# Performance work log

Measured on AMD Instinct MI355X. Metric: run time of the kernel, lower is better.

Reference implementation:

```python
import jax, jax.numpy as jnp
import numpy as np

DIM = 96
EPS = 1e-5

def setup_inputs() -> dict:
    key = jax.random.key(0)
    k1, k2, k3, k4 = jax.random.split(key, 4)
    x = jax.random.normal(k1, (2, DIM, 32, 64, 64), dtype=jnp.float32)
    # LayerNorm(8*dim) params and Linear(8*dim -> 2*dim, bias=False) weight
    gamma = jnp.ones((8 * DIM,), dtype=jnp.float32)
    beta = jnp.zeros((8 * DIM,), dtype=jnp.float32)
    w_red = jax.random.normal(k2, (8 * DIM, 2 * DIM), dtype=jnp.float32) * (1.0 / np.sqrt(8 * DIM))
    return {"x": x, "gamma": gamma, "beta": beta, "w_red": w_red}


def _patch_merge(x, gamma, beta, w_red):
    B, C, D, H, W = x.shape
    # pad trailing spatial dims to even (static shapes -> python ifs are fine)
    if (D % 2) or (H % 2) or (W % 2):
        x = jnp.pad(x, ((0, 0), (0, 0), (0, D % 2), (0, H % 2), (0, W % 2)))
    x = jnp.transpose(x, (0, 2, 3, 4, 1))  # B, D, H, W, C
    # gather the 8 octant sub-lattices and concat on channel
    parts = [x[:, d::2, h::2, w::2, :]
             for d in (0, 1) for h in (0, 1) for w in (0, 1)]
    # torch order: x0..x7 indexed by (d,h,w) bits with d slowest -> matches loop order
    y = jnp.concatenate(parts, axis=-1)  # B, D/2, H/2, W/2, 8C
    # LayerNorm over last dim
    mu = jnp.mean(y, axis=-1, keepdims=True)
    var = jnp.mean(jnp.square(y - mu), axis=-1, keepdims=True)
    y = (y - mu) * jax.lax.rsqrt(var + EPS) * gamma + beta
    # Linear 8C -> 2C, no bias
    y = jnp.einsum('bdhwc,co->bdhwo', y, w_red)
    return jnp.transpose(y, (0, 4, 1, 2, 3))  # B, 2C, D/2, H/2, W/2


def reference(x, gamma, beta, w_red):
    return _patch_merge(x, gamma, beta, w_red)
```

## Files before the change

kernel.cpp:

```cpp
#include <hip/hip_runtime.h>

typedef __attribute__((ext_vector_type(8))) short short8;
typedef __attribute__((ext_vector_type(4))) float float4v;

__device__ __forceinline__ unsigned short f2bf(float f) {
  unsigned int u = __float_as_uint(f);
  u += 0x7fffu + ((u >> 16) & 1u);
  return (unsigned short)(u >> 16);
}
__device__ __forceinline__ float bf2f(unsigned short h) {
  return __uint_as_float(((unsigned int)h) << 16);
}

__global__ __launch_bounds__(256)
void prep_kernel(const float* __restrict__ w_red, const float* __restrict__ gamma,
                 const float* __restrict__ beta, unsigned short* __restrict__ w_bf,
                 float* __restrict__ colsum, float* __restrict__ bias) {
  const int n = blockIdx.x;
  const int t = threadIdx.x;
  float cs = 0.f, bs = 0.f;
#pragma unroll
  for (int j = 0; j < 3; ++j) {
    int kp = j * 256 + t;
    int ko = (kp & 7) * 96 + (kp >> 3);
    float w = w_red[(size_t)ko * 192 + n];
    unsigned short v = f2bf(gamma[ko] * w);
    w_bf[(size_t)n * 768 + kp] = v;
    cs += bf2f(v);
    bs += beta[ko] * w;
  }
#pragma unroll
  for (int off = 1; off < 64; off <<= 1) {
    cs += __shfl_xor(cs, off, 64);
    bs += __shfl_xor(bs, off, 64);
  }
  __shared__ float red[2][4];
  const int wave = t >> 6;
  if ((t & 63) == 0) { red[0][wave] = cs; red[1][wave] = bs; }
  __syncthreads();
  if (t == 0) {
    colsum[n] = red[0][0] + red[0][1] + red[0][2] + red[0][3];
    bias[n]   = red[1][0] + red[1][1] + red[1][2] + red[1][3];
  }
}

__global__ __launch_bounds__(256, 6)
void pm_kernel(const float* __restrict__ x, const unsigned short* __restrict__ w_bf,
               const float* __restrict__ colsum, const float* __restrict__ bias,
               float* __restrict__ out) {
  __shared__ __align__(16) unsigned short Y[16][776];
  __shared__ float4 part4[4][8];
  __shared__ float smu[16], srs[16];

  const int tid = threadIdx.x;
  const int bid = blockIdx.x;
  const int b  = bid >> 10;
  const int dz = (bid >> 6) & 15;
  const int hy = (bid >> 1) & 31;
  const int wh = bid & 1;

  const float* xb = x + (size_t)b * 12582912u + (size_t)dz * 8192u
                      + (size_t)hy * 128u + wh * 32;

  const int r0 = tid >> 3;
  const int c0 = r0 >> 2;
  const int di = (r0 >> 1) & 1;
  const int hi = r0 & 1;
  const int w0 = (tid & 7) << 2;
  const float* xp = xb + (size_t)c0 * 131072u + di * 4096 + hi * 64 + w0;

  float4 v[12];
#pragma unroll
  for (int it = 0; it < 12; ++it)
    v[it] = *(const float4*)(xp + (size_t)it * 1048576u);

  const int lane = tid & 63;
  const int wave = tid >> 6;
  const int lrow = lane & 15;
  const int lq   = lane >> 4;

  const int wx0 = (tid & 7) << 1;
  const int k00 = c0 * 8 + di * 4 + hi * 2;
  float sum0 = 0.f, sq0 = 0.f, sum1 = 0.f, sq1 = 0.f;
#pragma unroll
  for (int it = 0; it < 12; ++it) {
    float4 vv = v[it];
    unsigned int p01 = (unsigned int)f2bf(vv.x) | ((unsigned int)f2bf(vv.y) << 16);
    unsigned int p23 = (unsigned int)f2bf(vv.z) | ((unsigned int)f2bf(vv.w) << 16);
    int k0 = it * 64 + k00;
    *(unsigned int*)&Y[wx0][k0]     = p01;
    *(unsigned int*)&Y[wx0 + 1][k0] = p23;
    sum0 += vv.x + vv.y;  sq0 += vv.x * vv.x + vv.y * vv.y;
    sum1 += vv.z + vv.w;  sq1 += vv.z * vv.z + vv.w * vv.w;
  }
#pragma unroll
  for (int off = 8; off < 64; off <<= 1) {
    sum0 += __shfl_xor(sum0, off, 64);  sq0 += __shfl_xor(sq0, off, 64);
    sum1 += __shfl_xor(sum1, off, 64);  sq1 += __shfl_xor(sq1, off, 64);
  }
  if (lane < 8) part4[wave][lane] = make_float4(sum0, sq0, sum1, sq1);

  const unsigned short* wrow[3];
#pragma unroll
  for (int t3 = 0; t3 < 3; ++t3)
    wrow[t3] = w_bf + (size_t)((wave * 3 + t3) * 16 + lrow) * 768 + lq * 8;
  short8 b0[3], b1[3];
#pragma unroll
  for (int t3 = 0; t3 < 3; ++t3) b0[t3] = *(const short8*)(wrow[t3]);
#pragma unroll
  for (int t3 = 0; t3 < 3; ++t3) b1[t3] = *(const short8*)(wrow[t3] + 32);

  __syncthreads();

  if (tid < 16) {
    int l = tid >> 1, odd = tid & 1;
    float s = 0.f, q = 0.f;
#pragma unroll
    for (int w = 0; w < 4; ++w) {
      float4 p = part4[w][l];
      s += odd ? p.z : p.x;
      q += odd ? p.w : p.y;
    }
    float mu  = s * (1.f / 768.f);
    float var = q * (1.f / 768.f) - mu * mu;
    smu[tid] = mu;
    srs[tid] = rsqrtf(var + 1e-5f);
  }

  float cs_n[3], bi_n[3];
#pragma unroll
  for (int t3 = 0; t3 < 3; ++t3) {
    int ng = (wave * 3 + t3) * 16 + lrow;
    cs_n[t3] = colsum[ng];
    bi_n[t3] = bias[ng];
  }

  __syncthreads();

  float4v acc[3];
#pragma unroll
  for (int j2 = 0; j2 < 3; ++j2)
#pragma unroll
    for (int r = 0; r < 4; ++r) acc[j2][r] = 0.f;

  for (int kc = 0; kc < 24; ++kc) {
    int kn = (kc + 2 <= 23) ? kc + 2 : 23;
    short8 b2[3];
#pragma unroll
    for (int t3 = 0; t3 < 3; ++t3) b2[t3] = *(const short8*)(wrow[t3] + kn * 32);
    short8 a0 = *(const short8*)&Y[lrow][kc * 32 + lq * 8];
#pragma unroll
    for (int t3 = 0; t3 < 3; ++t3)
      acc[t3] = __builtin_amdgcn_mfma_f32_16x16x32_bf16(a0, b0[t3], acc[t3], 0, 0, 0);
#pragma unroll
    for (int t3 = 0; t3 < 3; ++t3) { b0[t3] = b1[t3]; b1[t3] = b2[t3]; }
  }

  float4 mu4 = *(const float4*)&smu[lq * 4];
  float4 rs4 = *(const float4*)&srs[lq * 4];
  float* ob = out + (size_t)b * 3145728u + (size_t)dz * 1024u
                  + (size_t)hy * 32u + wh * 16 + lq * 4;
#pragma unroll
  for (int t3 = 0; t3 < 3; ++t3) {
    int ng = (wave * 3 + t3) * 16 + lrow;
    float4 vv;
    vv.x = rs4.x * (acc[t3][0] - mu4.x * cs_n[t3]) + bi_n[t3];
    vv.y = rs4.y * (acc[t3][1] - mu4.y * cs_n[t3]) + bi_n[t3];
    vv.z = rs4.z * (acc[t3][2] - mu4.z * cs_n[t3]) + bi_n[t3];
    vv.w = rs4.w * (acc[t3][3] - mu4.w * cs_n[t3]) + bi_n[t3];
    *(float4*)(ob + (size_t)ng * 16384u) = vv;
  }
}

extern "C" void kernel_launch(void* const* d_in, const int* in_sizes, int n_in,
                              void* d_out, int out_size, void* d_ws, size_t ws_size,
                              hipStream_t stream) {
  const float* x     = (const float*)d_in[0];
  const float* gamma = (const float*)d_in[1];
  const float* beta  = (const float*)d_in[2];
  const float* w_red = (const float*)d_in[3];
  float* out = (float*)d_out;

  unsigned short* w_bf = (unsigned short*)d_ws;
  float* colsum = (float*)((char*)d_ws + 294912);
  float* bias   = colsum + 192;

  prep_kernel<<<dim3(192), dim3(256), 0, stream>>>(w_red, gamma, beta, w_bf, colsum, bias);
  pm_kernel<<<dim3(2048), dim3(256), 0, stream>>>(x, w_bf, colsum, bias, out);
}
```

Measured before the change: 219.4 us.

## Pipeline x loads via global_load_lds with interleaved MFMA and fragment-ordered weights

Replaces the up-front register load of all 12 x chunks with a triple-buffered direct global-to-LDS pipeline. Each chunk is packed to bf16 in a swizzled double buffer and multiplied immediately by MFMA while the next chunks are in flight. Weights are pre-laid out in MFMA fragment order so B loads coalesce, and occupancy hints drop from 6 to 2 blocks per SM. The goal is to overlap HBM reads with conversion and matmul, at the cost of many per-chunk barriers and hand-written waitcnt logic that could be fragile.

```diff
diff --git a/kernel.cpp b/kernel.cpp
--- a/kernel.cpp
+++ b/kernel.cpp
@@ -11,13 +11,17 @@
 __device__ __forceinline__ float bf2f(unsigned short h) {
   return __uint_as_float(((unsigned int)h) << 16);
 }
+__device__ __forceinline__ unsigned int pack2bf(float a, float b) {
+  return (unsigned int)f2bf(a) | ((unsigned int)f2bf(b) << 16);
+}
 
 __global__ __launch_bounds__(256)
 void prep_kernel(const float* __restrict__ w_red, const float* __restrict__ gamma,
-                 const float* __restrict__ beta, unsigned short* __restrict__ w_bf,
+                 const float* __restrict__ beta, unsigned short* __restrict__ w_frag,
                  float* __restrict__ colsum, float* __restrict__ bias) {
   const int n = blockIdx.x;
   const int t = threadIdx.x;
+  const int ntile = n >> 4, lrow = n & 15;
   float cs = 0.f, bs = 0.f;
 #pragma unroll
   for (int j = 0; j < 3; ++j) {
@@ -25,7 +29,8 @@
     int ko = (kp & 7) * 96 + (kp >> 3);
     float w = w_red[(size_t)ko * 192 + n];
     unsigned short v = f2bf(gamma[ko] * w);
-    w_bf[(size_t)n * 768 + kp] = v;
+    int kc = kp >> 5, r = kp & 31, lq = r >> 3, e = r & 7;
+    w_frag[(size_t)((ntile * 24 + kc) * 64 + lq * 16 + lrow) * 8 + e] = v;
     cs += bf2f(v);
     bs += beta[ko] * w;
   }
@@ -44,11 +49,12 @@
   }
 }
 
-__global__ __launch_bounds__(256, 6)
-void pm_kernel(const float* __restrict__ x, const unsigned short* __restrict__ w_bf,
+__global__ __launch_bounds__(256, 2)
+void pm_kernel(const float* __restrict__ x, const unsigned short* __restrict__ w_frag,
                const float* __restrict__ colsum, const float* __restrict__ bias,
                float* __restrict__ out) {
-  __shared__ __align__(16) unsigned short Y[16][776];
+  __shared__ __align__(16) float F[3072];
+  __shared__ __align__(16) unsigned short Yb[2048];
   __shared__ float4 part4[4][8];
   __shared__ float smu[16], srs[16];
 
@@ -61,7 +67,6 @@
 
   const float* xb = x + (size_t)b * 12582912u + (size_t)dz * 8192u
                       + (size_t)hy * 128u + wh * 32;
-
   const int r0 = tid >> 3;
   const int c0 = r0 >> 2;
   const int di = (r0 >> 1) & 1;
@@ -69,47 +74,106 @@
   const int w0 = (tid & 7) << 2;
   const float* xp = xb + (size_t)c0 * 131072u + di * 4096 + hi * 64 + w0;
 
-  float4 v[12];
-#pragma unroll
-  for (int it = 0; it < 12; ++it)
-    v[it] = *(const float4*)(xp + (size_t)it * 1048576u);
-
   const int lane = tid & 63;
   const int wave = tid >> 6;
   const int lrow = lane & 15;
   const int lq   = lane >> 4;
 
+  char* ybase = (char*)Yb;
   const int wx0 = (tid & 7) << 1;
   const int k00 = c0 * 8 + di * 4 + hi * 2;
+  const int b0off = (wx0 * 128 + k00 * 2) ^ ((wx0 & 7) << 4);
+  const int b1off = ((wx0 + 1) * 128 + k00 * 2) ^ (((wx0 + 1) & 7) << 4);
+  const int ra0 = (lrow * 128 + lq * 16) ^ ((lrow & 7) << 4);
+  const int ra1 = (lrow * 128 + 64 + lq * 16) ^ ((lrow & 7) << 4);
+  const int fth = wave * 256 + lane * 4;
+  const int fwv = wave * 256;
+
+  const unsigned short* wb0 = w_frag + (size_t)(wave * 3 + 0) * 12288u + lane * 8;
+  const unsigned short* wb1 = w_frag + (size_t)(wave * 3 + 1) * 12288u + lane * 8;
+  const unsigned short* wb2 = w_frag + (size_t)(wave * 3 + 2) * 12288u + lane * 8;
+
+  short8 bA[6], bB[6];
+  float4v acc[3];
+#pragma unroll
+  for (int j = 0; j < 3; ++j)
+#pragma unroll
+    for (int r = 0; r < 4; ++r) acc[j][r] = 0.f;
   float sum0 = 0.f, sq0 = 0.f, sum1 = 0.f, sq1 = 0.f;
-#pragma unroll
-  for (int it = 0; it < 12; ++it) {
-    float4 vv = v[it];
-    unsigned int p01 = (unsigned int)f2bf(vv.x) | ((unsigned int)f2bf(vv.y) << 16);
-    unsigned int p23 = (unsigned int)f2bf(vv.z) | ((unsigned int)f2bf(vv.w) << 16);
-    int k0 = it * 64 + k00;
-    *(unsigned int*)&Y[wx0][k0]     = p01;
-    *(unsigned int*)&Y[wx0 + 1][k0] = p23;
-    sum0 += vv.x + vv.y;  sq0 += vv.x * vv.x + vv.y * vv.y;
-    sum1 += vv.z + vv.w;  sq1 += vv.z * vv.z + vv.w * vv.w;
-  }
+
+#define DMA(IT, SL)                                                            \
+  __builtin_amdgcn_global_load_lds(                                            \
+      (const __attribute__((address_space(1))) unsigned int*)(xp + (size_t)(IT) * 1048576u), \
+      (__attribute__((address_space(3))) unsigned int*)&F[(SL) * 1024 + fwv], 16, 0, 0)
+
+#define LOADB(BN, ITB)                                                         \
+  do {                                                                         \
+    const unsigned short* kp0 = wb0 + (ITB) * 1024;                            \
+    BN[0] = *(const short8*)(kp0);                                             \
+    BN[1] = *(const short8*)(kp0 + 512);                                       \
+    const unsigned short* kp1 = wb1 + (ITB) * 1024;                            \
+    BN[2] = *(const short8*)(kp1);                                             \
+    BN[3] = *(const short8*)(kp1 + 512);                                       \
+    const unsigned short* kp2 = wb2 + (ITB) * 1024;                            \
+    BN[4] = *(const short8*)(kp2);                                             \
+    BN[5] = *(const short8*)(kp2 + 512);                                       \
+  } while (0)
+
+#define PACK(SLP, PN)                                                          \
+  do {                                                                         \
+    float4 vv = *(const float4*)&F[(SLP) * 1024 + fth];                        \
+    *(unsigned int*)(ybase + (PN) * 2048 + b0off) = pack2bf(vv.x, vv.y);       \
+    *(unsigned int*)(ybase + (PN) * 2048 + b1off) = pack2bf(vv.z, vv.w);       \
+    sum0 += vv.x + vv.y;  sq0 += vv.x * vv.x + vv.y * vv.y;                    \
+    sum1 += vv.z + vv.w;  sq1 += vv.z * vv.z + vv.w * vv.w;                    \
+  } while (0)
+
+#define PHASE(IT, PC, PN, BC, BN, SLI, SLP)                                    \
+  do {                                                                         \
+    asm volatile("s_waitcnt lgkmcnt(0)" ::: "memory");                         \
+    __builtin_amdgcn_s_barrier();                                              \
+    { int itn = (IT) + 2 <= 11 ? (IT) + 2 : 11; DMA(itn, SLI); }               \
+    { int itb = (IT) + 1 <= 11 ? (IT) + 1 : 11; LOADB(BN, itb); }              \
+    asm volatile("s_waitcnt vmcnt(7)" ::: "memory");                           \
+    if ((IT) < 11) PACK(SLP, PN);                                              \
+    { short8 a0 = *(const short8*)(ybase + (PC) * 2048 + ra0);                 \
+      short8 a1 = *(const short8*)(ybase + (PC) * 2048 + ra1);                 \
+      acc[0] = __builtin_amdgcn_mfma_f32_16x16x32_bf16(a0, BC[0], acc[0], 0, 0, 0); \
+      acc[0] = __builtin_amdgcn_mfma_f32_16x16x32_bf16(a1, BC[1], acc[0], 0, 0, 0); \
+      acc[1] = __builtin_amdgcn_mfma_f32_16x16x32_bf16(a0, BC[2], acc[1], 0, 0, 0); \
+      acc[1] = __builtin_amdgcn_mfma_f32_16x16x32_bf16(a1, BC[3], acc[1], 0, 0, 0); \
+      acc[2] = __builtin_amdgcn_mfma_f32_16x16x32_bf16(a0, BC[4], acc[2], 0, 0, 0); \
+      acc[2] = __builtin_amdgcn_mfma_f32_16x16x32_bf16(a1, BC[5], acc[2], 0, 0, 0); } \
+  } while (0)
+
+  DMA(0, 0);
+  asm volatile("" ::: "memory");
+  DMA(1, 1);
+  asm volatile("" ::: "memory");
+  LOADB(bA, 0);
+  asm volatile("s_waitcnt vmcnt(7)" ::: "memory");
+  PACK(0, 0);
+
+#pragma unroll
+  for (int it6 = 0; it6 < 12; it6 += 6) {
+    PHASE(it6 + 0, 0, 1, bA, bB, 2, 1);
+    PHASE(it6 + 1, 1, 0, bB, bA, 0, 2);
+    PHASE(it6 + 2, 0, 1, bA, bB, 1, 0);
+    PHASE(it6 + 3, 1, 0, bB, bA, 2, 1);
+    PHASE(it6 + 4, 0, 1, bA, bB, 0, 2);
+    PHASE(it6 + 5, 1, 0, bB, bA, 1, 0);
+  }
+#undef PHASE
+#undef PACK
+#undef LOADB
+#undef DMA
+
 #pragma unroll
   for (int off = 8; off < 64; off <<= 1) {
     sum0 += __shfl_xor(sum0, off, 64);  sq0 += __shfl_xor(sq0, off, 64);
     sum1 += __shfl_xor(sum1, off, 64);  sq1 += __shfl_xor(sq1, off, 64);
   }
   if (lane < 8) part4[wave][lane] = make_float4(sum0, sq0, sum1, sq1);
-
-  const unsigned short* wrow[3];
-#pragma unroll
-  for (int t3 = 0; t3 < 3; ++t3)
-    wrow[t3] = w_bf + (size_t)((wave * 3 + t3) * 16 + lrow) * 768 + lq * 8;
-  short8 b0[3], b1[3];
-#pragma unroll
-  for (int t3 = 0; t3 < 3; ++t3) b0[t3] = *(const short8*)(wrow[t3]);
-#pragma unroll
-  for (int t3 = 0; t3 < 3; ++t3) b1[t3] = *(const short8*)(wrow[t3] + 32);
-
   __syncthreads();
 
   if (tid < 16) {
@@ -126,49 +190,22 @@
     smu[tid] = mu;
     srs[tid] = rsqrtf(var + 1e-5f);
   }
-
-  float cs_n[3], bi_n[3];
-#pragma unroll
-  for (int t3 = 0; t3 < 3; ++t3) {
-    int ng = (wave * 3 + t3) * 16 + lrow;
-    cs_n[t3] = colsum[ng];
-    bi_n[t3] = bias[ng];
-  }
-
   __syncthreads();
-
-  float4v acc[3];
-#pragma unroll
-  for (int j2 = 0; j2 < 3; ++j2)
-#pragma unroll
-    for (int r = 0; r < 4; ++r) acc[j2][r] = 0.f;
-
-  for (int kc = 0; kc < 24; ++kc) {
-    int kn = (kc + 2 <= 23) ? kc + 2 : 23;
-    short8 b2[3];
-#pragma unroll
-    for (int t3 = 0; t3 < 3; ++t3) b2[t3] = *(const short8*)(wrow[t3] + kn * 32);
-    short8 a0 = *(const short8*)&Y[lrow][kc * 32 + lq * 8];
-#pragma unroll
-    for (int t3 = 0; t3 < 3; ++t3)
-      acc[t3] = __builtin_amdgcn_mfma_f32_16x16x32_bf16(a0, b0[t3], acc[t3], 0, 0, 0);
-#pragma unroll
-    for (int t3 = 0; t3 < 3; ++t3) { b0[t3] = b1[t3]; b1[t3] = b2[t3]; }
-  }
 
   float4 mu4 = *(const float4*)&smu[lq * 4];
   float4 rs4 = *(const float4*)&srs[lq * 4];
   float* ob = out + (size_t)b * 3145728u + (size_t)dz * 1024u
                   + (size_t)hy * 32u + wh * 16 + lq * 4;
 #pragma unroll
-  for (int t3 = 0; t3 < 3; ++t3) {
-    int ng = (wave * 3 + t3) * 16 + lrow;
+  for (int j = 0; j < 3; ++j) {
+    int n = (wave * 3 + j) * 16 + lrow;
+    float cs = colsum[n], bi = bias[n];
     float4 vv;
-    vv.x = rs4.x * (acc[t3][0] - mu4.x * cs_n[t3]) + bi_n[t3];
-    vv.y = rs4.y * (acc[t3][1] - mu4.y * cs_n[t3]) + bi_n[t3];
-    vv.z = rs4.z * (acc[t3][2] - mu4.z * cs_n[t3]) + bi_n[t3];
-    vv.w = rs4.w * (acc[t3][3] - mu4.w * cs_n[t3]) + bi_n[t3];
-    *(float4*)(ob + (size_t)ng * 16384u) = vv;
+    vv.x = rs4.x * (acc[j][0] - mu4.x * cs) + bi;
+    vv.y = rs4.y * (acc[j][1] - mu4.y * cs) + bi;
+    vv.z = rs4.z * (acc[j][2] - mu4.z * cs) + bi;
+    vv.w = rs4.w * (acc[j][3] - mu4.w * cs) + bi;
+    *(float4*)(ob + (size_t)n * 16384u) = vv;
   }
 }
 
@@ -181,10 +218,10 @@
   const float* w_red = (const float*)d_in[3];
   float* out = (float*)d_out;
 
-  unsigned short* w_bf = (unsigned short*)d_ws;
+  unsigned short* w_frag = (unsigned short*)d_ws;
   float* colsum = (float*)((char*)d_ws + 294912);
   float* bias   = colsum + 192;
 
-  prep_kernel<<<dim3(192), dim3(256), 0, stream>>>(w_red, gamma, beta, w_bf, colsum, bias);
-  pm_kernel<<<dim3(2048), dim3(256), 0, stream>>>(x, w_bf, colsum, bias, out);
-}
+  prep_kernel<<<dim3(192), dim3(256), 0, stream>>>(w_red, gamma, beta, w_frag, colsum, bias);
+  pm_kernel<<<dim3(2048), dim3(256), 0, stream>>>(x, w_frag, colsum, bias, out);
+}
```

Result: faster. 197.3 us (-10.1%).
